# Optimization experiments

Measured on AMD Instinct MI355X. Metric: run time of the kernel, lower is better.

## Reference

```python
import jax, jax.numpy as jnp
import numpy as np

HID = 512
NOISE = 128
VOCAB = 5000
BATCH = 256
STEPS = 64
EPS = 1e-5
SOS = VOCAB - 1

def lrelu(x):
    return jnp.where(x >= 0, x, 0.2 * x)

def batchnorm(x, gamma, beta):
    # training-mode BatchNorm1d: batch statistics, biased variance
    mu = jnp.mean(x, axis=0)
    var = jnp.mean((x - mu) ** 2, axis=0)
    return gamma * (x - mu) / jnp.sqrt(var + EPS) + beta

def gru_cell(x, h, w_ih, w_hh, b_ih, b_hh):
    gi = x @ w_ih.T + b_ih  # [B, 3H]
    gh = h @ w_hh.T + b_hh
    i_r, i_z, i_n = jnp.split(gi, 3, axis=1)
    h_r, h_z, h_n = jnp.split(gh, 3, axis=1)
    r = jax.nn.sigmoid(i_r + h_r)
    zg = jax.nn.sigmoid(i_z + h_z)
    n = jnp.tanh(i_n + r * h_n)
    return (1.0 - zg) * n + zg * h

def setup_inputs() -> dict:
    key = jax.random.key(0)
    ks = jax.random.split(key, 12)
    s = lambda fi, fo: 1.0 / np.sqrt(fi)
    u = lambda k, shp, b: jax.random.uniform(k, shp, jnp.float32, -b, b)
    return {
        "z": jax.random.normal(ks[0], (BATCH, NOISE), jnp.float32),
        "z2h_w": u(ks[1], (HID, NOISE), s(NOISE, HID)),
        "z2h_b": u(ks[2], (HID,), s(NOISE, HID)),
        "emb": jax.random.normal(ks[3], (VOCAB, HID), jnp.float32),
        "bn1_g": jnp.ones((HID,), jnp.float32), "bn1_b": jnp.zeros((HID,), jnp.float32),
        "bn2_g": jnp.ones((2 * HID,), jnp.float32), "bn2_b": jnp.zeros((2 * HID,), jnp.float32),
        "bn3_g": jnp.ones((HID,), jnp.float32), "bn3_b": jnp.zeros((HID,), jnp.float32),
        "gru_wih": u(ks[4], (3 * HID, 2 * HID), s(HID, 0)),
        "gru_whh": u(ks[5], (3 * HID, HID), s(HID, 0)),
        "gru_bih": u(ks[6], (3 * HID,), s(HID, 0)),
        "gru_bhh": u(ks[7], (3 * HID,), s(HID, 0)),
        "h2o_w": u(ks[8], (VOCAB, HID), s(HID, 0)),
        "h2o_b": u(ks[9], (VOCAB,), s(HID, 0)),
        "gumbel_u": jax.random.uniform(ks[10], (STEPS, BATCH, VOCAB), jnp.float32),
        "num_steps": STEPS,
        "temperature": 0.8,
    }

def reference(z, z2h_w, z2h_b, emb, bn1_g, bn1_b, bn2_g, bn2_b, bn3_g, bn3_b,
              gru_wih, gru_whh, gru_bih, gru_bhh, h2o_w, h2o_b, gumbel_u,
              num_steps, temperature):
    z0 = batchnorm(lrelu(z @ z2h_w.T + z2h_b), bn1_g, bn1_b)  # [B, H]
    h0 = z0
    prev0 = jnp.full((z.shape[0],), SOS, jnp.int32)

    def step(carry, u_t):
        h, prev = carry
        e = lrelu(emb[prev])                                   # [B, H]
        si = batchnorm(jnp.concatenate([e, z0], axis=1), bn2_g, bn2_b)
        h = gru_cell(si, h, gru_wih, gru_whh, gru_bih, gru_bhh)
        o = batchnorm(lrelu(h), bn3_g, bn3_b)
        logits = o @ h2o_w.T + h2o_b                           # [B, V]
        g = -jnp.log(-jnp.log(u_t + 1e-20) + 1e-20)            # gumbel noise
        y = jax.nn.softmax((logits + g) / temperature, axis=-1)
        prev = jnp.argmax(y, axis=-1).astype(jnp.int32)
        return (h, prev), y

    _, ys = jax.lax.scan(step, (h0, prev0), gumbel_u[:num_steps])
    return jnp.transpose(ys, (1, 0, 2))  # [B, steps, V]
```

## Files before the change

### kernel.cpp

```cpp
#include <hip/hip_runtime.h>
#include <math.h>

#define HH 512
#define BB 256
#define NK 128

__device__ __forceinline__ float lrelu(float x){ return x >= 0.f ? x : 0.2f*x; }
__device__ __forceinline__ float sigm(float x){ return 1.f/(1.f+expf(-x)); }

__device__ __forceinline__ float blk_sum(float v, float* red){
  int t = threadIdx.x;
  red[t] = v; __syncthreads();
  #pragma unroll
  for (int s = 128; s > 0; s >>= 1){
    if (t < s) red[t] += red[t+s];
    __syncthreads();
  }
  float r = red[0]; __syncthreads();
  return r;
}

__global__ __launch_bounds__(256) void k_init(
    const float* __restrict__ z, const float* __restrict__ w, const float* __restrict__ bz,
    const float* __restrict__ g1, const float* __restrict__ b1,
    const float* __restrict__ g2, const float* __restrict__ b2,
    float* __restrict__ h0, float* __restrict__ sz0, int* __restrict__ prev, int sos)
{
  __shared__ float red[256];
  int j = blockIdx.x, i = threadIdx.x;
  const float4* zr = (const float4*)(z + i*NK);
  const float4* wr = (const float4*)(w + j*NK);
  float acc = bz[j];
  #pragma unroll 8
  for (int k = 0; k < NK/4; k++){
    float4 a = zr[k], b = wr[k];
    acc = fmaf(a.x, b.x, acc); acc = fmaf(a.y, b.y, acc);
    acc = fmaf(a.z, b.z, acc); acc = fmaf(a.w, b.w, acc);
  }
  float t = lrelu(acc);
  float mu  = blk_sum(t, red) * (1.f/BB);
  float d   = t - mu;
  float var = blk_sum(d*d, red) * (1.f/BB);
  float z0v = g1[j] * d / sqrtf(var + 1e-5f) + b1[j];
  h0[i*HH + j] = z0v;
  float mu2  = blk_sum(z0v, red) * (1.f/BB);
  float d2   = z0v - mu2;
  float var2 = blk_sum(d2*d2, red) * (1.f/BB);
  sz0[i*HH + j] = g2[HH + j] * d2 / sqrtf(var2 + 1e-5f) + b2[HH + j];
  if (j == 0) prev[i] = sos;
}

__global__ __launch_bounds__(256) void k_embed(
    const int* __restrict__ prev, const float* __restrict__ emb,
    const float* __restrict__ g2, const float* __restrict__ b2,
    float* __restrict__ se)
{
  __shared__ float red[256];
  int j = blockIdx.x, i = threadIdx.x;
  float t = lrelu(emb[prev[i]*HH + j]);
  float mu  = blk_sum(t, red) * (1.f/BB);
  float d   = t - mu;
  float var = blk_sum(d*d, red) * (1.f/BB);
  se[i*HH + j] = g2[j] * d / sqrtf(var + 1e-5f) + b2[j];
}

__global__ __launch_bounds__(256) void k_bn3(
    const float* __restrict__ h, const float* __restrict__ g3, const float* __restrict__ b3,
    float* __restrict__ o)
{
  __shared__ float red[256];
  int j = blockIdx.x, i = threadIdx.x;
  float t = lrelu(h[i*HH + j]);
  float mu  = blk_sum(t, red) * (1.f/BB);
  float d   = t - mu;
  float var = blk_sum(d*d, red) * (1.f/BB);
  o[i*HH + j] = g3[j] * d / sqrtf(var + 1e-5f) + b3[j];
}

#define KT 64
__global__ __launch_bounds__(256) void k_gru(
    const float* __restrict__ se, const float* __restrict__ hcur,
    const float* __restrict__ wih, const float* __restrict__ whh,
    const float* __restrict__ gz0, const float* __restrict__ bhh,
    float* __restrict__ hnext)
{
  __shared__ float sA[2][32][68];
  __shared__ float sB[6][16][68];
  int m0 = blockIdx.x*32, kc0 = blockIdx.y*16;
  int tl = threadIdx.x;
  float accI[3][2] = {{0,0},{0,0},{0,0}};
  float accH[3][2] = {{0,0},{0,0},{0,0}};
  int c = tl & 15, r2 = (tl >> 4) * 2;

  for (int kt = 0; kt < HH; kt += KT){
    #pragma unroll
    for (int rep = 0; rep < 4; rep++){
      int f = tl + 256*rep;
      int mat = f >> 9; int fi = f & 511;
      int row = fi >> 4; int kq = (fi & 15) * 4;
      const float* src = mat ? hcur : se;
      *(float4*)&sA[mat][row][kq] = *(const float4*)&src[(m0+row)*HH + kt + kq];
    }
    #pragma unroll
    for (int rep = 0; rep < 6; rep++){
      int f = tl + 256*rep;
      int m6 = f >> 8; int fi = f & 255;
      int row = fi >> 4; int kq = (fi & 15) * 4;
      int gate = (m6 < 3) ? m6 : m6 - 3;
      int n = gate*HH + kc0 + row;
      float4 v;
      if (m6 < 3) v = *(const float4*)&wih[n*1024 + kt + kq];
      else        v = *(const float4*)&whh[n*HH   + kt + kq];
      *(float4*)&sB[m6][row][kq] = v;
    }
    __syncthreads();
    #pragma unroll
    for (int kk = 0; kk < KT; kk += 4){
      float4 a0 = *(const float4*)&sA[0][r2  ][kk];
      float4 a1 = *(const float4*)&sA[0][r2+1][kk];
      float4 h0v = *(const float4*)&sA[1][r2  ][kk];
      float4 h1v = *(const float4*)&sA[1][r2+1][kk];
      #pragma unroll
      for (int g = 0; g < 3; g++){
        float4 we = *(const float4*)&sB[g][c][kk];
        accI[g][0] = fmaf(a0.x,we.x, fmaf(a0.y,we.y, fmaf(a0.z,we.z, fmaf(a0.w,we.w, accI[g][0]))));
        accI[g][1] = fmaf(a1.x,we.x, fmaf(a1.y,we.y, fmaf(a1.z,we.z, fmaf(a1.w,we.w, accI[g][1]))));
        float4 wh = *(const float4*)&sB[3+g][c][kk];
        accH[g][0] = fmaf(h0v.x,wh.x, fmaf(h0v.y,wh.y, fmaf(h0v.z,wh.z, fmaf(h0v.w,wh.w, accH[g][0]))));
        accH[g][1] = fmaf(h1v.x,wh.x, fmaf(h1v.y,wh.y, fmaf(h1v.z,wh.z, fmaf(h1v.w,wh.w, accH[g][1]))));
      }
    }
    __syncthreads();
  }
  int k = kc0 + c;
  #pragma unroll
  for (int r = 0; r < 2; r++){
    int i = m0 + r2 + r;
    float gir = accI[0][r] + gz0[i*1536 + k];
    float giz = accI[1][r] + gz0[i*1536 + 512 + k];
    float gin = accI[2][r] + gz0[i*1536 + 1024 + k];
    float ghr = accH[0][r] + bhh[k];
    float ghz = accH[1][r] + bhh[512 + k];
    float ghn = accH[2][r] + bhh[1024 + k];
    float rg = sigm(gir + ghr);
    float zg = sigm(giz + ghz);
    float ng = tanhf(gin + rg*ghn);
    float hv = hcur[i*HH + k];
    hnext[i*HH + k] = (1.f - zg)*ng + zg*hv;
  }
}

__global__ __launch_bounds__(256) void k_mm(
    const float* __restrict__ A, int lda,
    const float* __restrict__ Bm, int ldb,
    const float* __restrict__ bias, int N,
    float* __restrict__ out, int ldc,
    int mode,
    const float* __restrict__ gum, int ldg,
    const float* __restrict__ temp)
{
  __shared__ float sA[32][68];
  __shared__ float sB[64][68];
  int m0 = blockIdx.x*32, n0 = blockIdx.y*64;
  int tl = threadIdx.x;
  float acc[4][2] = {{0,0},{0,0},{0,0},{0,0}};
  int c1 = tl & 31, r4 = (tl >> 5) * 4;

  for (int kt = 0; kt < HH; kt += 64){
    #pragma unroll
    for (int rep = 0; rep < 2; rep++){
      int f = tl + 256*rep; int row = f >> 4; int kq = (f & 15) * 4;
      *(float4*)&sA[row][kq] = *(const float4*)&A[(m0+row)*lda + kt + kq];
    }
    #pragma unroll
    for (int rep = 0; rep < 4; rep++){
      int f = tl + 256*rep; int row = f >> 4; int kq = (f & 15) * 4;
      float4 v = make_float4(0.f,0.f,0.f,0.f);
      if (n0 + row < N) v = *(const float4*)&Bm[(n0+row)*ldb + kt + kq];
      *(float4*)&sB[row][kq] = v;
    }
    __syncthreads();
    #pragma unroll
    for (int kk = 0; kk < 64; kk += 4){
      float4 b0 = *(const float4*)&sB[c1     ][kk];
      float4 b1 = *(const float4*)&sB[c1 + 32][kk];
      #pragma unroll
      for (int r = 0; r < 4; r++){
        float4 a = *(const float4*)&sA[r4+r][kk];
        acc[r][0] = fmaf(a.x,b0.x, fmaf(a.y,b0.y, fmaf(a.z,b0.z, fmaf(a.w,b0.w, acc[r][0]))));
        acc[r][1] = fmaf(a.x,b1.x, fmaf(a.y,b1.y, fmaf(a.z,b1.z, fmaf(a.w,b1.w, acc[r][1]))));
      }
    }
    __syncthreads();
  }

  if (mode == 0){
    #pragma unroll
    for (int r = 0; r < 4; r++)
      #pragma unroll
      for (int j = 0; j < 2; j++){
        int v = n0 + c1 + 32*j;
        if (v < N) out[(m0+r4+r)*ldc + v] = acc[r][j] + bias[v];
      }
  } else {
    float tv = temp[0];
    #pragma unroll
    for (int r = 0; r < 4; r++)
      #pragma unroll
      for (int j = 0; j < 2; j++){
        int v = n0 + c1 + 32*j;
        if (v < N){
          int i = m0 + r4 + r;
          float u = gum[i*ldg + v];
          float g = -logf(-logf(u + 1e-20f) + 1e-20f);
          out[i*ldc + v] = (acc[r][j] + bias[v] + g) / tv;
        }
      }
  }
}

__global__ __launch_bounds__(256) void k_softmax(
    float* __restrict__ outrow, int ldc, int V, int* __restrict__ prev)
{
  __shared__ float sbuf[5000];
  __shared__ float rmax[256];
  __shared__ int   ridx[256];
  __shared__ float rsum[256];
  int i = blockIdx.x, t = threadIdx.x;
  float* row = outrow + (long)i*ldc;
  float bm = -3.4e38f; int bi = 0;
  for (int v = t; v < V; v += 256){
    float s = row[v]; sbuf[v] = s;
    if (s > bm){ bm = s; bi = v; }
  }
  rmax[t] = bm; ridx[t] = bi; __syncthreads();
  for (int s = 128; s > 0; s >>= 1){
    if (t < s){
      float mv = rmax[t+s]; int mi = ridx[t+s];
      if (mv > rmax[t] || (mv == rmax[t] && mi < ridx[t])){ rmax[t] = mv; ridx[t] = mi; }
    }
    __syncthreads();
  }
  float m = rmax[0];
  float ls = 0.f;
  for (int v = t; v < V; v += 256){
    float p = expf(sbuf[v] - m); sbuf[v] = p; ls += p;
  }
  rsum[t] = ls; __syncthreads();
  for (int s = 128; s > 0; s >>= 1){
    if (t < s) rsum[t] += rsum[t+s];
    __syncthreads();
  }
  float inv = 1.f / rsum[0];
  for (int v = t; v < V; v += 256) row[v] = sbuf[v] * inv;
  if (t == 0) prev[i] = ridx[0];
}

extern "C" void kernel_launch(void* const* d_in, const int* in_sizes, int n_in,
                              void* d_out, int out_size, void* d_ws, size_t ws_size,
                              hipStream_t stream)
{
  const float* z     = (const float*)d_in[0];
  const float* z2h_w = (const float*)d_in[1];
  const float* z2h_b = (const float*)d_in[2];
  const float* emb   = (const float*)d_in[3];
  const float* bn1_g = (const float*)d_in[4];
  const float* bn1_b = (const float*)d_in[5];
  const float* bn2_g = (const float*)d_in[6];
  const float* bn2_b = (const float*)d_in[7];
  const float* bn3_g = (const float*)d_in[8];
  const float* bn3_b = (const float*)d_in[9];
  const float* wih   = (const float*)d_in[10];
  const float* whh   = (const float*)d_in[11];
  const float* bih   = (const float*)d_in[12];
  const float* bhh   = (const float*)d_in[13];
  const float* h2o_w = (const float*)d_in[14];
  const float* h2o_b = (const float*)d_in[15];
  const float* gum   = (const float*)d_in[16];
  const float* temp  = (const float*)d_in[18];
  float* out = (float*)d_out;

  int V = in_sizes[15];
  int steps = out_size / (BB * V);

  char* ws = (char*)d_ws;
  float* sz0 = (float*)ws;  ws += (size_t)BB*HH*4;
  float* gz0 = (float*)ws;  ws += (size_t)BB*3*HH*4;
  float* se  = (float*)ws;  ws += (size_t)BB*HH*4;
  float* hb0 = (float*)ws;  ws += (size_t)BB*HH*4;
  float* hb1 = (float*)ws;  ws += (size_t)BB*HH*4;
  float* ob  = (float*)ws;  ws += (size_t)BB*HH*4;
  int*   prev = (int*)ws;

  k_init<<<HH, 256, 0, stream>>>(z, z2h_w, z2h_b, bn1_g, bn1_b, bn2_g, bn2_b,
                                 hb0, sz0, prev, V - 1);
  k_mm<<<dim3(BB/32, (3*HH)/64), 256, 0, stream>>>(
      sz0, HH, wih + HH, 2*HH, bih, 3*HH, gz0, 3*HH, 0, nullptr, 0, nullptr);

  for (int t = 0; t < steps; t++){
    const float* hc = (t & 1) ? hb1 : hb0;
    float*       hn = (t & 1) ? hb0 : hb1;
    k_embed<<<HH, 256, 0, stream>>>(prev, emb, bn2_g, bn2_b, se);
    k_gru<<<dim3(BB/32, HH/16), 256, 0, stream>>>(se, hc, wih, whh, gz0, bhh, hn);
    k_bn3<<<HH, 256, 0, stream>>>(hn, bn3_g, bn3_b, ob);
    k_mm<<<dim3(BB/32, (V + 63)/64), 256, 0, stream>>>(
        ob, HH, h2o_w, HH, h2o_b, V,
        out + (size_t)t*V, steps*V, 1, gum + (size_t)t*BB*V, V, temp);
    k_softmax<<<BB, 256, 0, stream>>>(out + (size_t)t*V, steps*V, V, prev);
  }
}
```

Baseline: 6.834 ms.

## Restructure recurrent step with transposed activations, split-K 128x128 GEMMs and fused cell+BN

Stores activations transposed (feature-major), replaces the GRU and vocab GEMMs with 128x128 register-tiled split-K kernels writing partial sums, and fuses the GRU gate math with the third batchnorm. The embedding batchnorm uses a one-pass sum and sum-of-squares reduction. Bias, gumbel noise and split-K reduction move into a vectorised softmax. It aims to raise per-thread compute reuse and cut launches and traffic, at the cost of extra partial-sum workspace and one-pass variance precision.

```diff
diff --git a/kernel.cpp b/kernel.cpp
--- a/kernel.cpp
+++ b/kernel.cpp
@@ -4,6 +4,8 @@
 #define HH 512
 #define BB 256
 #define NK 128
+#define G3 1536
+#define N6 3072
 
 __device__ __forceinline__ float lrelu(float x){ return x >= 0.f ? x : 0.2f*x; }
 __device__ __forceinline__ float sigm(float x){ return 1.f/(1.f+expf(-x)); }
@@ -17,6 +19,18 @@
     __syncthreads();
   }
   float r = red[0]; __syncthreads();
+  return r;
+}
+
+__device__ __forceinline__ float2 blk_sum2(float2 v, float2* red){
+  int t = threadIdx.x;
+  red[t] = v; __syncthreads();
+  #pragma unroll
+  for (int s = 128; s > 0; s >>= 1){
+    if (t < s){ red[t].x += red[t+s].x; red[t].y += red[t+s].y; }
+    __syncthreads();
+  }
+  float2 r = red[0]; __syncthreads();
   return r;
 }
 
@@ -24,7 +38,7 @@
     const float* __restrict__ z, const float* __restrict__ w, const float* __restrict__ bz,
     const float* __restrict__ g1, const float* __restrict__ b1,
     const float* __restrict__ g2, const float* __restrict__ b2,
-    float* __restrict__ h0, float* __restrict__ sz0, int* __restrict__ prev, int sos)
+    float* __restrict__ h0T, float* __restrict__ sz0, int* __restrict__ prev, int sos)
 {
   __shared__ float red[256];
   int j = blockIdx.x, i = threadIdx.x;
@@ -42,7 +56,7 @@
   float d   = t - mu;
   float var = blk_sum(d*d, red) * (1.f/BB);
   float z0v = g1[j] * d / sqrtf(var + 1e-5f) + b1[j];
-  h0[i*HH + j] = z0v;
+  h0T[j*BB + i] = z0v;
   float mu2  = blk_sum(z0v, red) * (1.f/BB);
   float d2   = z0v - mu2;
   float var2 = blk_sum(d2*d2, red) * (1.f/BB);
@@ -50,114 +64,11 @@
   if (j == 0) prev[i] = sos;
 }
 
-__global__ __launch_bounds__(256) void k_embed(
-    const int* __restrict__ prev, const float* __restrict__ emb,
-    const float* __restrict__ g2, const float* __restrict__ b2,
-    float* __restrict__ se)
-{
-  __shared__ float red[256];
-  int j = blockIdx.x, i = threadIdx.x;
-  float t = lrelu(emb[prev[i]*HH + j]);
-  float mu  = blk_sum(t, red) * (1.f/BB);
-  float d   = t - mu;
-  float var = blk_sum(d*d, red) * (1.f/BB);
-  se[i*HH + j] = g2[j] * d / sqrtf(var + 1e-5f) + b2[j];
-}
-
-__global__ __launch_bounds__(256) void k_bn3(
-    const float* __restrict__ h, const float* __restrict__ g3, const float* __restrict__ b3,
-    float* __restrict__ o)
-{
-  __shared__ float red[256];
-  int j = blockIdx.x, i = threadIdx.x;
-  float t = lrelu(h[i*HH + j]);
-  float mu  = blk_sum(t, red) * (1.f/BB);
-  float d   = t - mu;
-  float var = blk_sum(d*d, red) * (1.f/BB);
-  o[i*HH + j] = g3[j] * d / sqrtf(var + 1e-5f) + b3[j];
-}
-
-#define KT 64
-__global__ __launch_bounds__(256) void k_gru(
-    const float* __restrict__ se, const float* __restrict__ hcur,
-    const float* __restrict__ wih, const float* __restrict__ whh,
-    const float* __restrict__ gz0, const float* __restrict__ bhh,
-    float* __restrict__ hnext)
-{
-  __shared__ float sA[2][32][68];
-  __shared__ float sB[6][16][68];
-  int m0 = blockIdx.x*32, kc0 = blockIdx.y*16;
-  int tl = threadIdx.x;
-  float accI[3][2] = {{0,0},{0,0},{0,0}};
-  float accH[3][2] = {{0,0},{0,0},{0,0}};
-  int c = tl & 15, r2 = (tl >> 4) * 2;
-
-  for (int kt = 0; kt < HH; kt += KT){
-    #pragma unroll
-    for (int rep = 0; rep < 4; rep++){
-      int f = tl + 256*rep;
-      int mat = f >> 9; int fi = f & 511;
-      int row = fi >> 4; int kq = (fi & 15) * 4;
-      const float* src = mat ? hcur : se;
-      *(float4*)&sA[mat][row][kq] = *(const float4*)&src[(m0+row)*HH + kt + kq];
-    }
-    #pragma unroll
-    for (int rep = 0; rep < 6; rep++){
-      int f = tl + 256*rep;
-      int m6 = f >> 8; int fi = f & 255;
-      int row = fi >> 4; int kq = (fi & 15) * 4;
-      int gate = (m6 < 3) ? m6 : m6 - 3;
-      int n = gate*HH + kc0 + row;
-      float4 v;
-      if (m6 < 3) v = *(const float4*)&wih[n*1024 + kt + kq];
-      else        v = *(const float4*)&whh[n*HH   + kt + kq];
-      *(float4*)&sB[m6][row][kq] = v;
-    }
-    __syncthreads();
-    #pragma unroll
-    for (int kk = 0; kk < KT; kk += 4){
-      float4 a0 = *(const float4*)&sA[0][r2  ][kk];
-      float4 a1 = *(const float4*)&sA[0][r2+1][kk];
-      float4 h0v = *(const float4*)&sA[1][r2  ][kk];
-      float4 h1v = *(const float4*)&sA[1][r2+1][kk];
-      #pragma unroll
-      for (int g = 0; g < 3; g++){
-        float4 we = *(const float4*)&sB[g][c][kk];
-        accI[g][0] = fmaf(a0.x,we.x, fmaf(a0.y,we.y, fmaf(a0.z,we.z, fmaf(a0.w,we.w, accI[g][0]))));
-        accI[g][1] = fmaf(a1.x,we.x, fmaf(a1.y,we.y, fmaf(a1.z,we.z, fmaf(a1.w,we.w, accI[g][1]))));
-        float4 wh = *(const float4*)&sB[3+g][c][kk];
-        accH[g][0] = fmaf(h0v.x,wh.x, fmaf(h0v.y,wh.y, fmaf(h0v.z,wh.z, fmaf(h0v.w,wh.w, accH[g][0]))));
-        accH[g][1] = fmaf(h1v.x,wh.x, fmaf(h1v.y,wh.y, fmaf(h1v.z,wh.z, fmaf(h1v.w,wh.w, accH[g][1]))));
-      }
-    }
-    __syncthreads();
-  }
-  int k = kc0 + c;
-  #pragma unroll
-  for (int r = 0; r < 2; r++){
-    int i = m0 + r2 + r;
-    float gir = accI[0][r] + gz0[i*1536 + k];
-    float giz = accI[1][r] + gz0[i*1536 + 512 + k];
-    float gin = accI[2][r] + gz0[i*1536 + 1024 + k];
-    float ghr = accH[0][r] + bhh[k];
-    float ghz = accH[1][r] + bhh[512 + k];
-    float ghn = accH[2][r] + bhh[1024 + k];
-    float rg = sigm(gir + ghr);
-    float zg = sigm(giz + ghz);
-    float ng = tanhf(gin + rg*ghn);
-    float hv = hcur[i*HH + k];
-    hnext[i*HH + k] = (1.f - zg)*ng + zg*hv;
-  }
-}
-
 __global__ __launch_bounds__(256) void k_mm(
     const float* __restrict__ A, int lda,
     const float* __restrict__ Bm, int ldb,
     const float* __restrict__ bias, int N,
-    float* __restrict__ out, int ldc,
-    int mode,
-    const float* __restrict__ gum, int ldg,
-    const float* __restrict__ temp)
+    float* __restrict__ out, int ldc)
 {
   __shared__ float sA[32][68];
   __shared__ float sB[64][68];
@@ -193,33 +104,209 @@
     }
     __syncthreads();
   }
-
-  if (mode == 0){
-    #pragma unroll
-    for (int r = 0; r < 4; r++)
+  #pragma unroll
+  for (int r = 0; r < 4; r++)
+    #pragma unroll
+    for (int j = 0; j < 2; j++){
+      int v = n0 + c1 + 32*j;
+      if (v < N) out[(m0+r4+r)*ldc + v] = acc[r][j] + bias[v];
+    }
+}
+
+__global__ __launch_bounds__(256) void k_embed2(
+    const int* __restrict__ prev, const float* __restrict__ emb,
+    const float* __restrict__ g2, const float* __restrict__ b2,
+    float* __restrict__ seT)
+{
+  __shared__ float2 red[256];
+  int col = blockIdx.x, i = threadIdx.x;
+  float t = lrelu(emb[(size_t)prev[i]*HH + col]);
+  float2 sq = blk_sum2(make_float2(t, t*t), red);
+  float mu  = sq.x * (1.f/BB);
+  float var = sq.y * (1.f/BB) - mu*mu;
+  float sc  = g2[col] * rsqrtf(var + 1e-5f);
+  seT[col*BB + i] = fmaf(t, sc, b2[col] - mu*sc);
+}
+
+__global__ __launch_bounds__(256) void k_gru3(
+    const float* __restrict__ seT, const float* __restrict__ hT,
+    const float* __restrict__ wih, const float* __restrict__ whh,
+    float* __restrict__ gAllT, int Kb)
+{
+  __shared__ float sA[16][132];
+  __shared__ float sB[16][132];
+  const int tid = threadIdx.x;
+  const int rt = tid & 15, ct = tid >> 4;
+  const int m0 = blockIdx.x * 128;
+  const int n0 = blockIdx.y * 128;
+  const int k0 = blockIdx.z * Kb;
+  const bool hi = (n0 >= G3);
+  const float* __restrict__ XT = hi ? hT : seT;
+
+  float acc[8][8];
+  #pragma unroll
+  for (int r = 0; r < 8; r++)
+    #pragma unroll
+    for (int c = 0; c < 8; c++) acc[r][c] = 0.f;
+
+  const int am4 = (tid & 31) * 4, akk = tid >> 5;
+  const int bn  = tid & 127,     bkq = (tid >> 7)*4;
+
+  const int nkt = Kb >> 4;
+  for (int kt = 0; kt < nkt; kt++){
+    int kb = k0 + kt*16;
+    #pragma unroll
+    for (int p = 0; p < 2; p++){
+      int kk = akk + p*8;
+      *(float4*)&sA[kk][am4] = *(const float4*)&XT[(size_t)(kb + kk)*BB + m0 + am4];
+    }
+    {
+      int n = n0 + bn;
+      const float* Wr = hi ? (whh + (size_t)(n - G3)*HH) : (wih + (size_t)n*1024);
       #pragma unroll
-      for (int j = 0; j < 2; j++){
-        int v = n0 + c1 + 32*j;
-        if (v < N) out[(m0+r4+r)*ldc + v] = acc[r][j] + bias[v];
+      for (int p = 0; p < 2; p++){
+        int kq = bkq + p*8;
+        float4 v = *(const float4*)&Wr[kb + kq];
+        sB[kq+0][bn] = v.x; sB[kq+1][bn] = v.y;
+        sB[kq+2][bn] = v.z; sB[kq+3][bn] = v.w;
       }
-  } else {
-    float tv = temp[0];
-    #pragma unroll
-    for (int r = 0; r < 4; r++)
+    }
+    __syncthreads();
+    #pragma unroll
+    for (int kk = 0; kk < 16; kk++){
+      float4 a0 = *(const float4*)&sA[kk][rt*8];
+      float4 a1 = *(const float4*)&sA[kk][rt*8 + 4];
+      float4 b0 = *(const float4*)&sB[kk][ct*8];
+      float4 b1 = *(const float4*)&sB[kk][ct*8 + 4];
+      float av[8] = {a0.x,a0.y,a0.z,a0.w,a1.x,a1.y,a1.z,a1.w};
+      float bv[8] = {b0.x,b0.y,b0.z,b0.w,b1.x,b1.y,b1.z,b1.w};
       #pragma unroll
-      for (int j = 0; j < 2; j++){
-        int v = n0 + c1 + 32*j;
-        if (v < N){
-          int i = m0 + r4 + r;
-          float u = gum[i*ldg + v];
-          float g = -logf(-logf(u + 1e-20f) + 1e-20f);
-          out[i*ldc + v] = (acc[r][j] + bias[v] + g) / tv;
-        }
-      }
-  }
-}
-
-__global__ __launch_bounds__(256) void k_softmax(
+      for (int r = 0; r < 8; r++)
+        #pragma unroll
+        for (int c = 0; c < 8; c++)
+          acc[r][c] = fmaf(av[r], bv[c], acc[r][c]);
+    }
+    __syncthreads();
+  }
+
+  float* base = gAllT + (size_t)blockIdx.z * N6 * BB;
+  #pragma unroll
+  for (int c = 0; c < 8; c++){
+    int n = n0 + ct*8 + c;
+    float* dst = base + (size_t)n*BB + m0 + rt*8;
+    *(float4*)&dst[0] = make_float4(acc[0][c], acc[1][c], acc[2][c], acc[3][c]);
+    *(float4*)&dst[4] = make_float4(acc[4][c], acc[5][c], acc[6][c], acc[7][c]);
+  }
+}
+
+__global__ __launch_bounds__(256) void k_cell(
+    const float* __restrict__ gAllT, int KS,
+    const float* __restrict__ gz0, const float* __restrict__ bhh,
+    const float* __restrict__ hcT,
+    const float* __restrict__ g3, const float* __restrict__ b3,
+    float* __restrict__ hnT, float* __restrict__ oT)
+{
+  __shared__ float2 red[256];
+  int col = blockIdx.x, i = threadIdx.x;
+  float giR=0.f, giZ=0.f, giN=0.f, ghR=0.f, ghZ=0.f, ghN=0.f;
+  for (int ks = 0; ks < KS; ks++){
+    const float* b = gAllT + (size_t)ks * N6 * BB;
+    giR += b[(size_t)(       col)*BB + i];
+    giZ += b[(size_t)( HH  + col)*BB + i];
+    giN += b[(size_t)(2*HH + col)*BB + i];
+    ghR += b[(size_t)(G3       + col)*BB + i];
+    ghZ += b[(size_t)(G3 +  HH + col)*BB + i];
+    ghN += b[(size_t)(G3 + 2*HH + col)*BB + i];
+  }
+  const float* gz = gz0 + (size_t)i*G3;
+  float rg = sigm(giR + gz[col]        + ghR + bhh[col]);
+  float zg = sigm(giZ + gz[HH + col]   + ghZ + bhh[HH + col]);
+  float ng = tanhf(giN + gz[2*HH + col] + rg*(ghN + bhh[2*HH + col]));
+  float hv = hcT[col*BB + i];
+  float hn = (1.f - zg)*ng + zg*hv;
+  hnT[col*BB + i] = hn;
+  float t3 = lrelu(hn);
+  float2 sq = blk_sum2(make_float2(t3, t3*t3), red);
+  float mu  = sq.x * (1.f/BB);
+  float var = sq.y * (1.f/BB) - mu*mu;
+  float sc  = g3[col] * rsqrtf(var + 1e-5f);
+  oT[col*BB + i] = fmaf(t3, sc, b3[col] - mu*sc);
+}
+
+__global__ __launch_bounds__(256) void k_mm3(
+    const float* __restrict__ oT, const float* __restrict__ W, int V,
+    float* __restrict__ pm, int Kb)
+{
+  __shared__ float sA[16][132];
+  __shared__ float sB[16][132];
+  const int tid = threadIdx.x;
+  const int rt = tid & 15, ct = tid >> 4;
+  const int m0 = blockIdx.x * 128;
+  const int n0 = blockIdx.y * 128;
+  const int k0 = blockIdx.z * Kb;
+
+  float acc[8][8];
+  #pragma unroll
+  for (int r = 0; r < 8; r++)
+    #pragma unroll
+    for (int c = 0; c < 8; c++) acc[r][c] = 0.f;
+
+  const int am4 = (tid & 31) * 4, akk = tid >> 5;
+  const int bn  = tid & 127,     bkq = (tid >> 7)*4;
+  int nrow = n0 + bn; if (nrow >= V) nrow = V - 1;
+  const float* Wr = W + (size_t)nrow*HH;
+
+  const int nkt = Kb >> 4;
+  for (int kt = 0; kt < nkt; kt++){
+    int kb = k0 + kt*16;
+    #pragma unroll
+    for (int p = 0; p < 2; p++){
+      int kk = akk + p*8;
+      *(float4*)&sA[kk][am4] = *(const float4*)&oT[(size_t)(kb + kk)*BB + m0 + am4];
+    }
+    #pragma unroll
+    for (int p = 0; p < 2; p++){
+      int kq = bkq + p*8;
+      float4 v = *(const float4*)&Wr[kb + kq];
+      sB[kq+0][bn] = v.x; sB[kq+1][bn] = v.y;
+      sB[kq+2][bn] = v.z; sB[kq+3][bn] = v.w;
+    }
+    __syncthreads();
+    #pragma unroll
+    for (int kk = 0; kk < 16; kk++){
+      float4 a0 = *(const float4*)&sA[kk][rt*8];
+      float4 a1 = *(const float4*)&sA[kk][rt*8 + 4];
+      float4 b0 = *(const float4*)&sB[kk][ct*8];
+      float4 b1 = *(const float4*)&sB[kk][ct*8 + 4];
+      float av[8] = {a0.x,a0.y,a0.z,a0.w,a1.x,a1.y,a1.z,a1.w};
+      float bv[8] = {b0.x,b0.y,b0.z,b0.w,b1.x,b1.y,b1.z,b1.w};
+      #pragma unroll
+      for (int r = 0; r < 8; r++)
+        #pragma unroll
+        for (int c = 0; c < 8; c++)
+          acc[r][c] = fmaf(av[r], bv[c], acc[r][c]);
+    }
+    __syncthreads();
+  }
+
+  float* base = pm + (size_t)blockIdx.z * BB * V;
+  #pragma unroll
+  for (int r = 0; r < 8; r++){
+    int i = m0 + rt*8 + r;
+    float* dst = base + (size_t)i*V;
+    #pragma unroll
+    for (int g = 0; g < 2; g++){
+      int v4 = n0 + ct*8 + g*4;
+      if (v4 < V)
+        *(float4*)&dst[v4] = make_float4(acc[r][g*4], acc[r][g*4+1], acc[r][g*4+2], acc[r][g*4+3]);
+    }
+  }
+}
+
+__global__ __launch_bounds__(256) void k_softmax2(
+    const float* __restrict__ pm, int KS,
+    const float* __restrict__ bias,
+    const float* __restrict__ gum, const float* __restrict__ temp,
     float* __restrict__ outrow, int ldc, int V, int* __restrict__ prev)
 {
   __shared__ float sbuf[5000];
@@ -227,11 +314,26 @@
   __shared__ int   ridx[256];
   __shared__ float rsum[256];
   int i = blockIdx.x, t = threadIdx.x;
-  float* row = outrow + (long)i*ldc;
+  float invT = 1.f / temp[0];
+  const float* gp = gum + (size_t)i*V;
   float bm = -3.4e38f; int bi = 0;
-  for (int v = t; v < V; v += 256){
-    float s = row[v]; sbuf[v] = s;
-    if (s > bm){ bm = s; bi = v; }
+  for (int v = 4*t; v < V; v += 1024){
+    float4 zz = make_float4(0.f,0.f,0.f,0.f);
+    for (int ks = 0; ks < KS; ks++){
+      float4 p = *(const float4*)&pm[((size_t)ks*BB + i)*V + v];
+      zz.x += p.x; zz.y += p.y; zz.z += p.z; zz.w += p.w;
+    }
+    float4 bv = *(const float4*)&bias[v];
+    float4 u  = *(const float4*)&gp[v];
+    zz.x = (zz.x + bv.x - logf(-logf(u.x + 1e-20f) + 1e-20f)) * invT;
+    zz.y = (zz.y + bv.y - logf(-logf(u.y + 1e-20f) + 1e-20f)) * invT;
+    zz.z = (zz.z + bv.z - logf(-logf(u.z + 1e-20f) + 1e-20f)) * invT;
+    zz.w = (zz.w + bv.w - logf(-logf(u.w + 1e-20f) + 1e-20f)) * invT;
+    *(float4*)&sbuf[v] = zz;
+    if (zz.x > bm){ bm = zz.x; bi = v;   }
+    if (zz.y > bm){ bm = zz.y; bi = v+1; }
+    if (zz.z > bm){ bm = zz.z; bi = v+2; }
+    if (zz.w > bm){ bm = zz.w; bi = v+3; }
   }
   rmax[t] = bm; ridx[t] = bi; __syncthreads();
   for (int s = 128; s > 0; s >>= 1){
@@ -243,8 +345,12 @@
   }
   float m = rmax[0];
   float ls = 0.f;
-  for (int v = t; v < V; v += 256){
-    float p = expf(sbuf[v] - m); sbuf[v] = p; ls += p;
+  for (int v = 4*t; v < V; v += 1024){
+    float4 zz = *(const float4*)&sbuf[v];
+    zz.x = expf(zz.x - m); zz.y = expf(zz.y - m);
+    zz.z = expf(zz.z - m); zz.w = expf(zz.w - m);
+    *(float4*)&sbuf[v] = zz;
+    ls += zz.x + zz.y + zz.z + zz.w;
   }
   rsum[t] = ls; __syncthreads();
   for (int s = 128; s > 0; s >>= 1){
@@ -252,7 +358,12 @@
     __syncthreads();
   }
   float inv = 1.f / rsum[0];
-  for (int v = t; v < V; v += 256) row[v] = sbuf[v] * inv;
+  float* row = outrow + (size_t)i*ldc;
+  for (int v = 4*t; v < V; v += 1024){
+    float4 zz = *(const float4*)&sbuf[v];
+    zz.x *= inv; zz.y *= inv; zz.z *= inv; zz.w *= inv;
+    *(float4*)&row[v] = zz;
+  }
   if (t == 0) prev[i] = ridx[0];
 }
 
@@ -283,29 +394,46 @@
   int V = in_sizes[15];
   int steps = out_size / (BB * V);
 
+  size_t fixed = (size_t)BB*HH*4
+               + (size_t)BB*G3*4
+               + (size_t)HH*BB*4*4
+               + 1024;
+  int cand[4][2] = {{8,4},{4,2},{2,1},{1,1}};
+  int ksg = 1, ksm = 1;
+  for (int c = 0; c < 4; c++){
+    size_t need = fixed + (size_t)cand[c][0]*N6*BB*4 + (size_t)cand[c][1]*BB*V*4;
+    if (need <= ws_size){ ksg = cand[c][0]; ksm = cand[c][1]; break; }
+  }
+
   char* ws = (char*)d_ws;
   float* sz0 = (float*)ws;  ws += (size_t)BB*HH*4;
-  float* gz0 = (float*)ws;  ws += (size_t)BB*3*HH*4;
-  float* se  = (float*)ws;  ws += (size_t)BB*HH*4;
-  float* hb0 = (float*)ws;  ws += (size_t)BB*HH*4;
-  float* hb1 = (float*)ws;  ws += (size_t)BB*HH*4;
-  float* ob  = (float*)ws;  ws += (size_t)BB*HH*4;
+  float* gz0 = (float*)ws;  ws += (size_t)BB*G3*4;
+  float* seT = (float*)ws;  ws += (size_t)HH*BB*4;
+  float* hT0 = (float*)ws;  ws += (size_t)HH*BB*4;
+  float* hT1 = (float*)ws;  ws += (size_t)HH*BB*4;
+  float* oT  = (float*)ws;  ws += (size_t)HH*BB*4;
+  float* gAllT = (float*)ws; ws += (size_t)ksg*N6*BB*4;
+  float* pm  = (float*)ws;  ws += (size_t)ksm*BB*V*4;
   int*   prev = (int*)ws;
 
   k_init<<<HH, 256, 0, stream>>>(z, z2h_w, z2h_b, bn1_g, bn1_b, bn2_g, bn2_b,
-                                 hb0, sz0, prev, V - 1);
-  k_mm<<<dim3(BB/32, (3*HH)/64), 256, 0, stream>>>(
-      sz0, HH, wih + HH, 2*HH, bih, 3*HH, gz0, 3*HH, 0, nullptr, 0, nullptr);
+                                 hT0, sz0, prev, V - 1);
+  k_mm<<<dim3(BB/32, G3/64), 256, 0, stream>>>(
+      sz0, HH, wih + HH, 2*HH, bih, G3, gz0, G3);
+
+  int Kb_g = HH / ksg;
+  int Kb_m = HH / ksm;
+  int nb_v = (V + 127) / 128;
 
   for (int t = 0; t < steps; t++){
-    const float* hc = (t & 1) ? hb1 : hb0;
-    float*       hn = (t & 1) ? hb0 : hb1;
-    k_embed<<<HH, 256, 0, stream>>>(prev, emb, bn2_g, bn2_b, se);
-    k_gru<<<dim3(BB/32, HH/16), 256, 0, stream>>>(se, hc, wih, whh, gz0, bhh, hn);
-    k_bn3<<<HH, 256, 0, stream>>>(hn, bn3_g, bn3_b, ob);
-    k_mm<<<dim3(BB/32, (V + 63)/64), 256, 0, stream>>>(
-        ob, HH, h2o_w, HH, h2o_b, V,
-        out + (size_t)t*V, steps*V, 1, gum + (size_t)t*BB*V, V, temp);
-    k_softmax<<<BB, 256, 0, stream>>>(out + (size_t)t*V, steps*V, V, prev);
-  }
-}
+    const float* hc = (t & 1) ? hT1 : hT0;
+    float*       hn = (t & 1) ? hT0 : hT1;
+    k_embed2<<<HH, 256, 0, stream>>>(prev, emb, bn2_g, bn2_b, seT);
+    k_gru3<<<dim3(2, N6/128, ksg), 256, 0, stream>>>(seT, hc, wih, whh, gAllT, Kb_g);
+    k_cell<<<HH, 256, 0, stream>>>(gAllT, ksg, gz0, bhh, hc, bn3_g, bn3_b, hn, oT);
+    k_mm3<<<dim3(2, nb_v, ksm), 256, 0, stream>>>(oT, h2o_w, V, pm, Kb_m);
+    k_softmax2<<<BB, 256, 0, stream>>>(pm, ksm, h2o_b,
+                                       gum + (size_t)t*BB*V, temp,
+                                       out + (size_t)t*V, steps*V, V, prev);
+  }
+}
```

Result: faster. 5.936 ms (-13.1%).
